# Kernel optimization log

Measured on AMD Instinct MI355X. Metric: run time of the kernel, lower is better.

## Reference

```python
import jax, jax.numpy as jnp
import numpy as np

# ProbLog program semantics, closed-form:
# Grid 2x2, cell index = 2*X + Y: 0=(0,0), 1=(0,1), 2=(1,0), 3=(1,1).
# Actions (query order): 0=stay, 1=up, 2=down, 3=left, 4=right.
# transition/5 only defines clauses for stay/up/down (plus west/east which never
# unify with left/right), so left/right can never produce 'unsafe'.
# unsafe :- pacman(X,Y), action(A), transition(X,Y,A,X1,Y1), ghost(X1,Y1).
# evidence(safe) conditions the action query: P(a|safe) = p_a(a)*safe(a)/sum.

def _build_T():
    T = np.zeros((5, 4, 4), dtype=np.float32)  # [action, pac_cell, ghost_cell]
    for c in range(4):
        T[0, c, c] = 1.0  # stay
    # up: (x,y)->(x,y+1): cell0->1, cell2->3 (y=1 cells move off-grid -> no ghost)
    T[1, 0, 1] = 1.0
    T[1, 2, 3] = 1.0
    # down: (x,y)->(x,y-1): cell1->0, cell3->2
    T[2, 1, 0] = 1.0
    T[2, 3, 2] = 1.0
    # left/right: no transition clauses -> always safe
    return T

_T = _build_T()


def setup_inputs() -> dict:
    key = jax.random.key(0)
    ks = jax.random.split(key, 4)
    B, H = 16384, 2048
    s = 1.0 / np.sqrt(H)
    return {
        "x": jax.random.normal(ks[0], (B, H), dtype=jnp.float32),
        "Wg": jax.random.normal(ks[1], (H, 4), dtype=jnp.float32) * s,
        "bg": jnp.zeros((4,), dtype=jnp.float32),
        "Wp": jax.random.normal(ks[2], (H, 4), dtype=jnp.float32) * s,
        "bp": jnp.zeros((4,), dtype=jnp.float32),
        "Wa": jax.random.normal(ks[3], (H, 5), dtype=jnp.float32) * s,
        "ba": jnp.zeros((5,), dtype=jnp.float32),
    }


def reference(x, Wg, bg, Wp, bp, Wa, ba):
    ghost = jax.nn.softmax(x @ Wg + bg, axis=-1)   # [B,4]
    pacman = jax.nn.softmax(x @ Wp + bp, axis=-1)  # [B,4]
    base = jax.nn.softmax(x @ Wa + ba, axis=-1)    # [B,5]
    T = jnp.asarray(_T)                            # [5,4,4]
    # P(unsafe | action=a) = sum_c pac[c] * ghost[target(c,a)]
    unsafe = jnp.einsum('bc,acd,bd->ba', pacman, T, ghost)  # [B,5]
    joint = base * (1.0 - unsafe)                  # P(action=a, safe)
    return joint / jnp.sum(joint, axis=-1, keepdims=True)   # P(action=a | safe)
```

## Files before the change

kernel.cpp:

```cpp
#include <hip/hip_runtime.h>


typedef __fp16 h2_t __attribute__((ext_vector_type(2)));
typedef __fp16 h4_t __attribute__((ext_vector_type(4)));
typedef __fp16 h8_t __attribute__((ext_vector_type(8)));
typedef float f32x4 __attribute__((ext_vector_type(4)));

__global__ void pack_bfrag(const float* __restrict__ Wg,
                           const float* __restrict__ Wp,
                           const float* __restrict__ Wa,
                           h8_t* __restrict__ bfrag)
{
    const int t = blockIdx.x * 256 + threadIdx.x;
    const int iter = t >> 6, lane = t & 63;
    const int n = lane & 15, kg = lane >> 4;
    h8_t v;
    #pragma unroll
    for (int j = 0; j < 8; ++j) {
        const int k = iter * 32 + kg * 8 + j;
        float f;
        if (n < 4)       f = Wg[k * 4 + n];
        else if (n < 8)  f = Wp[k * 4 + (n - 4)];
        else if (n < 13) f = Wa[k * 5 + (n - 8)];
        else             f = 0.f;
        v[j] = (__fp16)f;
    }
    bfrag[t] = v;
}

__global__ __launch_bounds__(256, 2)
void gemm_mfma(const float* __restrict__ x,
               const h8_t* __restrict__ bfrag,
               const float* __restrict__ bg, const float* __restrict__ bp,
               const float* __restrict__ ba, float* __restrict__ out)
{
    __shared__ float dt[2][2][16][17];

    const int tid = threadIdx.x;
    const int w   = tid >> 6;
    const int l   = tid & 63;
    const int rt2 = w & 1;
    const int ks  = w >> 1;
    const int row0 = blockIdx.x * 32 + rt2 * 16;
    const int m  = l & 15;
    const int kg = l >> 4;

    const float4* xg = (const float4*)x;
    const long base = (long)(row0 + m) * 512 + ks * 256 + kg * 2;
    const h8_t* bf = bfrag + (ks * 32) * 64 + l;

    float4 pa[4], pb[4];
    h8_t   pf[4];
    #pragma unroll
    for (int d = 0; d < 4; ++d) {
        pa[d] = xg[base + d * 8];
        pb[d] = xg[base + d * 8 + 1];
        pf[d] = bf[d * 64];
    }

    f32x4 acc = {0.f, 0.f, 0.f, 0.f};

    #pragma unroll 4
    for (int i = 0; i < 32; ++i) {
        const int s = i & 3;
        const float4 xa = pa[s], xb = pb[s];
        const h8_t b8 = pf[s];
        if (i + 4 < 32) {
            pa[s] = xg[base + (i + 4) * 8];
            pb[s] = xg[base + (i + 4) * 8 + 1];
            pf[s] = bf[(i + 4) * 64];
        }
        const h2_t a01 = __builtin_amdgcn_cvt_pkrtz(xa.x, xa.y);
        const h2_t a23 = __builtin_amdgcn_cvt_pkrtz(xa.z, xa.w);
        const h2_t a45 = __builtin_amdgcn_cvt_pkrtz(xb.x, xb.y);
        const h2_t a67 = __builtin_amdgcn_cvt_pkrtz(xb.z, xb.w);
        const h4_t alo = __builtin_shufflevector(a01, a23, 0, 1, 2, 3);
        const h4_t ahi = __builtin_shufflevector(a45, a67, 0, 1, 2, 3);
        const h8_t a8  = __builtin_shufflevector(alo, ahi, 0, 1, 2, 3, 4, 5, 6, 7);
        acc = __builtin_amdgcn_mfma_f32_16x16x32_f16(a8, b8, acc, 0, 0, 0);
    }

    #pragma unroll
    for (int r = 0; r < 4; ++r)
        dt[rt2][ks][kg * 4 + r][m] = acc[r];
    __syncthreads();

    if (w < 2 && l < 16) {
        float lg[13];
        #pragma unroll
        for (int c = 0; c < 13; ++c)
            lg[c] = dt[w][0][l][c] + dt[w][1][l][c];

        const float g0 = lg[0] + bg[0], g1 = lg[1] + bg[1], g2 = lg[2] + bg[2], g3 = lg[3] + bg[3];
        const float q0 = lg[4] + bp[0], q1 = lg[5] + bp[1], q2 = lg[6] + bp[2], q3 = lg[7] + bp[3];
        const float a0 = lg[8] + ba[0], a1 = lg[9] + ba[1], a2 = lg[10] + ba[2],
                    a3 = lg[11] + ba[3], a4 = lg[12] + ba[4];

        float mx, sum, inv;
        mx = fmaxf(fmaxf(g0, g1), fmaxf(g2, g3));
        const float eg0 = __expf(g0 - mx), eg1 = __expf(g1 - mx), eg2 = __expf(g2 - mx), eg3 = __expf(g3 - mx);
        sum = eg0 + eg1 + eg2 + eg3; inv = 1.f / sum;
        const float G0 = eg0 * inv, G1 = eg1 * inv, G2 = eg2 * inv, G3 = eg3 * inv;

        mx = fmaxf(fmaxf(q0, q1), fmaxf(q2, q3));
        const float ep0 = __expf(q0 - mx), ep1 = __expf(q1 - mx), ep2 = __expf(q2 - mx), ep3 = __expf(q3 - mx);
        sum = ep0 + ep1 + ep2 + ep3; inv = 1.f / sum;
        const float P0 = ep0 * inv, P1 = ep1 * inv, P2 = ep2 * inv, P3 = ep3 * inv;

        mx = fmaxf(fmaxf(fmaxf(a0, a1), fmaxf(a2, a3)), a4);
        const float ea0 = __expf(a0 - mx), ea1 = __expf(a1 - mx), ea2 = __expf(a2 - mx),
                    ea3 = __expf(a3 - mx), ea4 = __expf(a4 - mx);
        sum = ea0 + ea1 + ea2 + ea3 + ea4; inv = 1.f / sum;
        const float A0 = ea0 * inv, A1 = ea1 * inv, A2 = ea2 * inv, A3 = ea3 * inv, A4 = ea4 * inv;

        const float u0 = P0 * G0 + P1 * G1 + P2 * G2 + P3 * G3;
        const float u1 = P0 * G1 + P2 * G3;
        const float u2 = P1 * G0 + P3 * G2;

        const float j0 = A0 * (1.f - u0), j1 = A1 * (1.f - u1), j2 = A2 * (1.f - u2),
                    j3 = A3, j4 = A4;
        const float isd = 1.f / (j0 + j1 + j2 + j3 + j4);

        float* o = out + (long)(row0 + l) * 5;
        o[0] = j0 * isd; o[1] = j1 * isd; o[2] = j2 * isd; o[3] = j3 * isd; o[4] = j4 * isd;
    }
}

extern "C" void kernel_launch(void* const* d_in, const int* in_sizes, int n_in,
                              void* d_out, int out_size, void* d_ws, size_t ws_size,
                              hipStream_t stream) {
    const float* x  = (const float*)d_in[0];
    const float* Wg = (const float*)d_in[1];
    const float* bg = (const float*)d_in[2];
    const float* Wp = (const float*)d_in[3];
    const float* bp = (const float*)d_in[4];
    const float* Wa = (const float*)d_in[5];
    const float* ba = (const float*)d_in[6];
    float* out = (float*)d_out;

    h8_t* bfrag = (h8_t*)d_ws;

    pack_bfrag<<<16, 256, 0, stream>>>(Wg, Wp, Wa, bfrag);
    gemm_mfma<<<512, 256, 0, stream>>>(x, bfrag, bg, bp, ba, out);
}
```

Baseline: 208.0 us.

## Stage x tiles through double-buffered LDS with coalesced nontemporal row loads

Each block now loads 32 rows of x in 256-column chunks as fully coalesced per-row float4 reads (nontemporal), stores them into a padded double-buffered LDS tile, and the MFMA waves read their A fragments from LDS. The chunk start is staggered by block index so concurrent blocks hit different column ranges. This replaces strided per-lane global reads, aiming at better DRAM coalescing for this bandwidth-bound GEMV-like pass. It adds about 66KB of LDS per block, which may cut occupancy below the 2-block launch bound, plus a barrier per chunk.

```diff
diff --git a/kernel.cpp b/kernel.cpp
--- a/kernel.cpp
+++ b/kernel.cpp
@@ -5,6 +5,8 @@
 typedef __fp16 h4_t __attribute__((ext_vector_type(4)));
 typedef __fp16 h8_t __attribute__((ext_vector_type(8)));
 typedef float f32x4 __attribute__((ext_vector_type(4)));
+
+#define ROWSTRIDE 260
 
 __global__ void pack_bfrag(const float* __restrict__ Wg,
                            const float* __restrict__ Wp,
@@ -34,6 +36,7 @@
                const float* __restrict__ bg, const float* __restrict__ bp,
                const float* __restrict__ ba, float* __restrict__ out)
 {
+    __shared__ float cbuf[2][32 * ROWSTRIDE];
     __shared__ float dt[2][2][16][17];
 
     const int tid = threadIdx.x;
@@ -41,43 +44,70 @@
     const int l   = tid & 63;
     const int rt2 = w & 1;
     const int ks  = w >> 1;
-    const int row0 = blockIdx.x * 32 + rt2 * 16;
+    const int row0 = blockIdx.x * 32;
     const int m  = l & 15;
     const int kg = l >> 4;
 
-    const float4* xg = (const float4*)x;
-    const long base = (long)(row0 + m) * 512 + ks * 256 + kg * 2;
-    const h8_t* bf = bfrag + (ks * 32) * 64 + l;
+    const int cc0 = blockIdx.x & 7;
 
-    float4 pa[4], pb[4];
-    h8_t   pf[4];
-    #pragma unroll
-    for (int d = 0; d < 4; ++d) {
-        pa[d] = xg[base + d * 8];
-        pb[d] = xg[base + d * 8 + 1];
-        pf[d] = bf[d * 64];
+    const long srow = (long)(row0 + w * 8);
+    f32x4 sr[8];
+
+    {
+        const int cc = cc0;
+        #pragma unroll
+        for (int rr = 0; rr < 8; ++rr)
+            sr[rr] = __builtin_nontemporal_load(
+                (const f32x4*)(x + (srow + rr) * 2048 + cc * 256 + l * 4));
+        #pragma unroll
+        for (int rr = 0; rr < 8; ++rr)
+            *(f32x4*)&cbuf[0][(w * 8 + rr) * ROWSTRIDE + l * 4] = sr[rr];
     }
 
     f32x4 acc = {0.f, 0.f, 0.f, 0.f};
+    const int arow = (rt2 * 16 + m) * ROWSTRIDE;
 
-    #pragma unroll 4
-    for (int i = 0; i < 32; ++i) {
-        const int s = i & 3;
-        const float4 xa = pa[s], xb = pb[s];
-        const h8_t b8 = pf[s];
-        if (i + 4 < 32) {
-            pa[s] = xg[base + (i + 4) * 8];
-            pb[s] = xg[base + (i + 4) * 8 + 1];
-            pf[s] = bf[(i + 4) * 64];
+    for (int c = 0; c < 8; ++c) {
+        const int cc = (cc0 + c) & 7;
+
+        h8_t b8[4];
+        #pragma unroll
+        for (int t = 0; t < 4; ++t)
+            b8[t] = bfrag[(cc * 8 + ks * 4 + t) * 64 + l];
+
+        const int ccn = (cc0 + c + 1) & 7;
+        if (c + 1 < 8) {
+            #pragma unroll
+            for (int rr = 0; rr < 8; ++rr)
+                sr[rr] = __builtin_nontemporal_load(
+                    (const f32x4*)(x + (srow + rr) * 2048 + ccn * 256 + l * 4));
         }
-        const h2_t a01 = __builtin_amdgcn_cvt_pkrtz(xa.x, xa.y);
-        const h2_t a23 = __builtin_amdgcn_cvt_pkrtz(xa.z, xa.w);
-        const h2_t a45 = __builtin_amdgcn_cvt_pkrtz(xb.x, xb.y);
-        const h2_t a67 = __builtin_amdgcn_cvt_pkrtz(xb.z, xb.w);
-        const h4_t alo = __builtin_shufflevector(a01, a23, 0, 1, 2, 3);
-        const h4_t ahi = __builtin_shufflevector(a45, a67, 0, 1, 2, 3);
-        const h8_t a8  = __builtin_shufflevector(alo, ahi, 0, 1, 2, 3, 4, 5, 6, 7);
-        acc = __builtin_amdgcn_mfma_f32_16x16x32_f16(a8, b8, acc, 0, 0, 0);
+
+        __syncthreads();
+
+        const float* cb = cbuf[c & 1];
+        #pragma unroll
+        for (int t = 0; t < 4; ++t) {
+            const int sl = ks * 4 + t;
+            const int off = arow + sl * 32 + kg * 8;
+            const f32x4 v0 = *(const f32x4*)&cb[off];
+            const f32x4 v1 = *(const f32x4*)&cb[off + 4];
+            const h2_t a01 = __builtin_amdgcn_cvt_pkrtz(v0.x, v0.y);
+            const h2_t a23 = __builtin_amdgcn_cvt_pkrtz(v0.z, v0.w);
+            const h2_t a45 = __builtin_amdgcn_cvt_pkrtz(v1.x, v1.y);
+            const h2_t a67 = __builtin_amdgcn_cvt_pkrtz(v1.z, v1.w);
+            const h4_t alo = __builtin_shufflevector(a01, a23, 0, 1, 2, 3);
+            const h4_t ahi = __builtin_shufflevector(a45, a67, 0, 1, 2, 3);
+            const h8_t a8  = __builtin_shufflevector(alo, ahi, 0, 1, 2, 3, 4, 5, 6, 7);
+            acc = __builtin_amdgcn_mfma_f32_16x16x32_f16(a8, b8[t], acc, 0, 0, 0);
+        }
+
+        if (c + 1 < 8) {
+            float* nb = cbuf[(c + 1) & 1];
+            #pragma unroll
+            for (int rr = 0; rr < 8; ++rr)
+                *(f32x4*)&nb[(w * 8 + rr) * ROWSTRIDE + l * 4] = sr[rr];
+        }
     }
 
     #pragma unroll
@@ -121,7 +151,7 @@
                     j3 = A3, j4 = A4;
         const float isd = 1.f / (j0 + j1 + j2 + j3 + j4);
 
-        float* o = out + (long)(row0 + l) * 5;
+        float* o = out + (long)(row0 + w * 16 + l) * 5;
         o[0] = j0 * isd; o[1] = j1 * isd; o[2] = j2 * isd; o[3] = j3 * isd; o[4] = j4 * isd;
     }
 }
```

After: 200.6 us. 3.5% less time.
